# Kernel tuning notes

Hardware: AMD Instinct MI355X
Metric: run time of the kernel (lower is better)

## Reference

```python
import jax, jax.numpy as jnp
import numpy as np

jax.config.update('jax_enable_x64', True)

NV = 300000
NT = 1200000

# Lookup tables from GshellHelper buffers
TRIANGLE_TABLE = jnp.asarray(np.array([
    [-1, -1, -1, -1, -1, -1], [1, 0, 2, -1, -1, -1], [4, 0, 3, -1, -1, -1],
    [1, 4, 2, 1, 3, 4], [3, 1, 5, -1, -1, -1], [2, 3, 0, 2, 5, 3],
    [1, 4, 0, 1, 5, 4], [4, 2, 5, -1, -1, -1], [4, 5, 2, -1, -1, -1],
    [4, 1, 0, 4, 5, 1], [3, 2, 0, 3, 5, 2], [1, 3, 5, -1, -1, -1],
    [4, 1, 2, 4, 3, 1], [3, 0, 4, -1, -1, -1], [2, 0, 1, -1, -1, -1],
    [-1, -1, -1, -1, -1, -1]], dtype=np.int64))
NUM_TRIANGLES_TABLE = jnp.asarray(np.array([0, 1, 1, 2, 1, 2, 2, 1, 1, 2, 2, 1, 2, 1, 1, 0], dtype=np.int64))
BASE_TET_EDGES = jnp.asarray(np.array([0, 1, 0, 2, 0, 3, 1, 2, 1, 3, 2, 3], dtype=np.int64))


def setup_inputs() -> dict:
    key = jax.random.key(0)
    k1, k2, k3 = jax.random.split(key, 3)
    pos_nx3 = jax.random.normal(k1, (NV, 3), dtype=jnp.float32)
    sdf_n = jax.random.normal(k2, (NV,), dtype=jnp.float32)
    tet_fx4 = jax.random.randint(k3, (NT, 4), 0, NV, dtype=jnp.int64)
    return {'pos_nx3': pos_nx3, 'sdf_n': sdf_n, 'tet_fx4': tet_fx4}


def _marching_tets(pos_nx3, sdf_n, tet_fx4):
    Nv = pos_nx3.shape[0]
    Nt = tet_fx4.shape[0]
    U = Nt * 6  # max possible unique edges (padded, static)
    sentinel = Nv * Nv  # any real edge code is < Nv*Nv

    occ_n = sdf_n > 0                               # [Nv]
    occ_fx4 = occ_n[tet_fx4]                        # [Nt,4]

    # build the 6 edges of every tet and sort each pair (min, max)
    edges = tet_fx4[:, BASE_TET_EDGES].reshape(-1, 2)   # [Nt*6, 2]
    e0 = jnp.minimum(edges[:, 0], edges[:, 1])
    e1 = jnp.maximum(edges[:, 0], edges[:, 1])
    code = e0 * Nv + e1                                  # [Nt*6] int64 edge key

    # dedup edges (torch.unique(..., return_inverse=True) equivalent, padded)
    uniq, inv = jnp.unique(code, size=U, fill_value=sentinel, return_inverse=True)
    u0 = jnp.clip(uniq // Nv, 0, Nv - 1)
    u1 = jnp.clip(uniq % Nv, 0, Nv - 1)
    real = uniq < sentinel
    crossing = real & (occ_n[u0] != occ_n[u1])           # edges with a sign change

    # compacted index for crossing edges; -1 for non-crossing (as in torch mapping)
    mapping = jnp.where(crossing, jnp.cumsum(crossing.astype(jnp.int64)) - 1, -1)
    idx_map = mapping[inv].reshape(Nt, 6)                # [Nt,6]

    # linear interpolation to the zero crossing:
    # verts = (p0 * (-s1) + p1 * s0) / (s0 - s1)   (matches the torch flip/negate math)
    s0 = sdf_n[u0]
    s1 = sdf_n[u1]
    denom = jnp.where(crossing, s0 - s1, jnp.asarray(1.0, sdf_n.dtype))
    v = (pos_nx3[u0] * (-s1 / denom)[:, None] + pos_nx3[u1] * (s0 / denom)[:, None])

    # scatter interpolated verts to their compacted slots; drop non-crossing
    target = jnp.where(crossing, mapping, U)
    verts = jnp.zeros((U, 3), pos_nx3.dtype).at[target].set(v, mode='drop')

    # per-tet sign pattern -> triangle table lookup
    v_id = jnp.asarray([1, 2, 4, 8], dtype=jnp.int64)
    tetindex = (occ_fx4.astype(jnp.int64) * v_id[None, :]).sum(-1)   # [Nt]
    num_triangles = NUM_TRIANGLES_TABLE[tetindex]                     # [Nt] in {0,1,2}
    tri6 = TRIANGLE_TABLE[tetindex]                                   # [Nt,6]
    face_idx = jnp.take_along_axis(idx_map, jnp.clip(tri6, 0, 5), axis=1).reshape(Nt, 2, 3)
    valid_tri = jnp.arange(2, dtype=jnp.int64)[None, :] < num_triangles[:, None]
    faces = jnp.where(valid_tri[:, :, None], face_idx, -1)            # [Nt,2,3], -1 padded

    return verts, faces, num_triangles, crossing


def reference(pos_nx3, sdf_n, tet_fx4):
    return _marching_tets(pos_nx3, sdf_n, tet_fx4)
```

## Files before the change

### kernel.cpp

```cpp
#include <hip/hip_runtime.h>
#include <stdint.h>

typedef unsigned long long u64;
typedef unsigned int u32;

#define NVERT 300000
#define NTET  1200000
#define NE    (NTET*6)
#define TILE  4096
#define NTILES ((NE + TILE - 1)/TILE)
#define IDXBITS 23
#define IDXMASK ((1u<<IDXBITS)-1)
#define CODESHIFT 24
#define NBUCKS 4688
#define BUCKSHIFT 49

#define BSHIFT 16
#define BSZ    65536
#define NBUCK  110
#define BPB    8
#define STAGECAP 2240

#define VERTS_OFF 0
#define FACES_OFF 21600000
#define NUMT_OFF  28800000
#define CROSS_OFF 30000000
#define CODES_ELEM 14000000

__constant__ int c_ea[6] = {0,0,0,1,1,2};
__constant__ int c_eb[6] = {1,2,3,2,3,3};
__constant__ int c_numtri[16] = {0,1,1,2,1,2,2,1,1,2,2,1,2,1,1,0};
__constant__ int c_tritab[16][6] = {
 {-1,-1,-1,-1,-1,-1},{1,0,2,-1,-1,-1},{4,0,3,-1,-1,-1},{1,4,2,1,3,4},
 {3,1,5,-1,-1,-1},{2,3,0,2,5,3},{1,4,0,1,5,4},{4,2,5,-1,-1,-1},
 {4,5,2,-1,-1,-1},{4,1,0,4,5,1},{3,2,0,3,5,2},{1,3,5,-1,-1,-1},
 {4,1,2,4,3,1},{3,0,4,-1,-1,-1},{2,0,1,-1,-1,-1},{-1,-1,-1,-1,-1,-1}};

__device__ __forceinline__ int sw(int j){ return j ^ ((j >> 4) & 15); }

__global__ void k_pack(const int* __restrict__ tet, const float* __restrict__ sdf,
                       u64* __restrict__ dst, float* __restrict__ occF, u32* __restrict__ hist){
  __shared__ u32 h[NBUCKS];
  int tid = threadIdx.x;
  for (int r=tid; r<NBUCKS; r+=256) h[r]=0;
  __syncthreads();
  int t = blockIdx.x*blockDim.x + tid;
  if (t < NTET){
    int4 q = ((const int4*)tet)[t];
    int v[4] = {q.x, q.y, q.z, q.w};
    u32 o[4];
    int occ = 0;
    #pragma unroll
    for (int j=0;j<4;j++){ o[j] = sdf[v[j]] > 0.f ? 1u : 0u; occ |= (int)o[j] << j; }
    occF[t] = (float)occ;
    u64 base = (u64)t*6;
    #pragma unroll
    for (int k=0;k<6;k++){
      int a = v[c_ea[k]], b = v[c_eb[k]];
      u64 cross = (o[c_ea[k]] != o[c_eb[k]]) ? 1ull : 0ull;
      int e0 = min(a,b), e1 = max(a,b);
      u64 code = ((u64)e0 << 19) | (u64)e1;
      u64 key = (code << CODESHIFT) | (cross << IDXBITS) | (base + (u64)k);
      dst[base+k] = key;
      atomicAdd(&h[(u32)(key >> BUCKSHIFT)], 1u);
    }
  }
  __syncthreads();
  for (int r=tid; r<NBUCKS; r+=256){
    u32 c = h[r];
    if (c) atomicAdd(&hist[r], c);
  }
}

__global__ void k_psd(const float* __restrict__ pos, const float* __restrict__ sdf,
                      float4* __restrict__ psd){
  int v = blockIdx.x*blockDim.x + threadIdx.x;
  if (v < NVERT) psd[v] = make_float4(pos[3*v], pos[3*v+1], pos[3*v+2], sdf[v]);
}

__global__ void k_fillm1(float4* __restrict__ p, int n4){
  int i = blockIdx.x*blockDim.x + threadIdx.x;
  if (i < n4) p[i] = make_float4(-1.f,-1.f,-1.f,-1.f);
}

__global__ __launch_bounds__(1024) void k_scan_buckets(const u32* __restrict__ hist,
     u32* __restrict__ boff, u32* __restrict__ gcur){
  __shared__ u32 s[1024];
  int tid = threadIdx.x;
  u32 carry = 0;
  for (int start=0; start<NBUCKS; start+=1024){
    int idx = start + tid;
    u32 x = (idx < NBUCKS) ? hist[idx] : 0;
    s[tid] = x; __syncthreads();
    for (int off=1; off<1024; off<<=1){
      u32 t = (tid >= off) ? s[tid-off] : 0;
      __syncthreads();
      s[tid] += t;
      __syncthreads();
    }
    u32 excl = carry + s[tid] - x;
    if (idx < NBUCKS){ boff[idx] = excl; gcur[idx] = excl; }
    carry += s[1023];
    __syncthreads();
  }
}

__global__ __launch_bounds__(256) void k_bucket_scatter(const u64* __restrict__ src,
     u64* __restrict__ dst, u32* __restrict__ gcur){
  __shared__ u32 cnt[NBUCKS];
  __shared__ u32 cur[NBUCKS];
  int tid = threadIdx.x;
  for (int r=tid;r<NBUCKS;r+=256) cnt[r]=0;
  __syncthreads();
  int gi = blockIdx.x*TILE + tid*16;
  u64 kk[16];
  if (gi + 16 <= NE){
    const ulonglong2* p2 = (const ulonglong2*)(src + gi);
    #pragma unroll
    for (int k2=0;k2<8;k2++){ ulonglong2 t = p2[k2]; kk[2*k2]=t.x; kk[2*k2+1]=t.y; }
  } else {
    #pragma unroll
    for (int k=0;k<16;k++) kk[k] = (gi+k < NE) ? src[gi+k] : 0ull;
  }
  #pragma unroll
  for (int k=0;k<16;k++){
    if (gi+k < NE) atomicAdd(&cnt[(u32)(kk[k] >> BUCKSHIFT)], 1u);
  }
  __syncthreads();
  for (int r=tid;r<NBUCKS;r+=256){
    u32 c = cnt[r];
    cur[r] = c ? atomicAdd(&gcur[r], c) : 0u;
  }
  __syncthreads();
  #pragma unroll
  for (int k=0;k<16;k++){
    if (gi+k < NE){
      u32 b = (u32)(kk[k] >> BUCKSHIFT);
      u32 p = atomicAdd(&cur[b], 1u);
      dst[p] = kk[k];
    }
  }
}

__global__ __launch_bounds__(256) void k_sort_bucket(const u64* __restrict__ src,
     u64* __restrict__ dst, const u32* __restrict__ hist, const u32* __restrict__ boff){
  __shared__ u64 keys[TILE];
  __shared__ u64 wsum[4];
  int b = blockIdx.x, tid = threadIdx.x;
  u32 n = hist[b];
  if (n == 0) return;
  u32 base = boff[b];
  for (int k=0;k<16;k++){
    int j = k*256 + tid;
    keys[sw(j)] = (j < (int)n) ? src[base + j] : ~0ull;
  }
  __syncthreads();
  for (int q=0;q<26;q+=2){
    int sh = 24 + q;
    u64 myk[16];
    u32 vpack = 0;
    u64 c = 0;
    #pragma unroll
    for (int k=0;k<16;k++){
      myk[k] = keys[sw(tid*16+k)];
      u32 d2 = (u32)((myk[k] >> sh) & 3);
      vpack |= d2 << (2*k);
      c += 1ull << (16*d2);
    }
    u64 v = c;
    #pragma unroll
    for (int off=1; off<64; off<<=1){
      u64 t = __shfl_up(v, off, 64);
      if ((tid & 63) >= off) v += t;
    }
    if ((tid & 63) == 63) wsum[tid >> 6] = v;
    __syncthreads();
    u64 pre = 0, tot = 0;
    #pragma unroll
    for (int wv=0; wv<4; wv++){
      u64 wsv = wsum[wv];
      if (wv < (tid >> 6)) pre += wsv;
      tot += wsv;
    }
    u64 run = v + pre - c;
    u32 T0=(u32)(tot&0xFFFF), T1=(u32)((tot>>16)&0xFFFF), T2=(u32)((tot>>32)&0xFFFF);
    u64 Bp = ((u64)(T0) << 16) | ((u64)(T0+T1) << 32) | ((u64)(T0+T1+T2) << 48);
    #pragma unroll
    for (int k=0;k<16;k++){
      u32 d2 = (vpack >> (2*k)) & 3;
      u32 pos = (u32)((Bp >> (16*d2)) & 0xFFFF) + (u32)((run >> (16*d2)) & 0xFFFF);
      run += 1ull << (16*d2);
      keys[sw((int)pos)] = myk[k];
    }
    __syncthreads();
  }
  for (int k=0;k<16;k++){
    int j = k*256 + tid;
    if (j < (int)n) dst[base + j] = keys[sw(j)];
  }
}

__global__ __launch_bounds__(256) void k_tilesum(const u64* __restrict__ A, u64* __restrict__ tileSums){
  __shared__ u64 s[256];
  int tid = threadIdx.x;
  int start = blockIdx.x*TILE + tid*16;
  u64 myk[16];
  if (start < NE){
    const ulonglong2* A2 = (const ulonglong2*)(A + start);
    #pragma unroll
    for (int k2=0;k2<8;k2++){ ulonglong2 t = A2[k2]; myk[2*k2]=t.x; myk[2*k2+1]=t.y; }
  } else {
    #pragma unroll
    for (int k=0;k<16;k++) myk[k]=0;
  }
  u64 prev = (start > 0 && start <= NE) ? A[start-1] : ~0ull;
  u32 th=0, tc=0;
  #pragma unroll
  for (int k=0;k<16;k++){
    int i = start + k;
    if (i < NE){
      u64 v = myk[k];
      if ((v>>CODESHIFT) != (prev>>CODESHIFT)){
        th++;
        if ((v>>IDXBITS) & 1ull) tc++;
      }
      prev = v;
    }
  }
  s[tid] = ((u64)th<<32) | (u64)tc;
  __syncthreads();
  for (int off=128; off>0; off>>=1){
    if (tid<off) s[tid]+=s[tid+off];
    __syncthreads();
  }
  if (tid==0) tileSums[blockIdx.x] = s[0];
}

__global__ void k_scan_tiles(u64* __restrict__ tileSums, u64* __restrict__ tileOff){
  __shared__ u64 s[256];
  int tid = threadIdx.x;
  u64 carry=0;
  for (int start=0; start<NTILES; start+=256){
    int idx=start+tid;
    u64 x = (idx<NTILES)? tileSums[idx] : 0;
    s[tid]=x; __syncthreads();
    for (int off=1;off<256;off<<=1){
      u64 t=(tid>=off)?s[tid-off]:0;
      __syncthreads();
      s[tid]+=t;
      __syncthreads();
    }
    u64 incl=s[tid], tot=s[255];
    if (idx<NTILES) tileOff[idx] = carry + incl - x;
    carry += tot;
    __syncthreads();
  }
  if (tid==0) tileOff[NTILES] = carry;
}

__global__ __launch_bounds__(256) void k_emit_light(const u64* __restrict__ A,
     const u64* __restrict__ tileOff, u64* __restrict__ pairs, u32* __restrict__ cursors,
     u64* __restrict__ codes, float* __restrict__ crossing_out){
  __shared__ u64 s[256];
  __shared__ u32 cnt[NBUCK], lcur[NBUCK];
  __shared__ u32 lofs[NBUCK+1];
  __shared__ u32 gbase[NBUCK];
  __shared__ u32 pscan[128];
  __shared__ u64 stage[STAGECAP];
  int tid=threadIdx.x, blk=blockIdx.x;
  int start = blk*TILE + tid*16;
  if (tid < NBUCK){ cnt[tid]=0; lcur[tid]=0; }
  u64 myk[16];
  if (start < NE){
    const ulonglong2* A2 = (const ulonglong2*)(A + start);
    #pragma unroll
    for (int k2=0;k2<8;k2++){ ulonglong2 t = A2[k2]; myk[2*k2]=t.x; myk[2*k2+1]=t.y; }
  } else {
    #pragma unroll
    for (int k=0;k<16;k++) myk[k]=0;
  }
  u64 prev = (start > 0 && start <= NE) ? A[start-1] : ~0ull;
  u32 headm=0, crossm=0;
  #pragma unroll
  for (int k=0;k<16;k++){
    int i = start + k;
    if (i<NE){
      u64 v = myk[k];
      if ((v>>CODESHIFT) != (prev>>CODESHIFT)) headm |= 1u<<k;
      if ((v>>IDXBITS) & 1ull) crossm |= 1u<<k;
      prev = v;
    }
  }
  __syncthreads();
  #pragma unroll
  for (int k=0;k<16;k++){
    if ((start+k) < NE && ((crossm>>k)&1u))
      atomicAdd(&cnt[((u32)myk[k] & IDXMASK)>>BSHIFT], 1u);
  }
  u32 th = __popc(headm), tc = __popc(headm & crossm);
  u64 x = ((u64)th<<32)|(u64)tc;
  s[tid]=x; __syncthreads();
  for (int off=1;off<256;off<<=1){
    u64 t=(tid>=off)?s[tid-off]:0;
    __syncthreads();
    s[tid]+=t;
    __syncthreads();
  }
  u64 excl = s[tid]-x;
  if (tid < 128) pscan[tid] = (tid < NBUCK) ? cnt[tid] : 0;
  __syncthreads();
  for (int off=1; off<128; off<<=1){
    u32 t = 0;
    if (tid < 128 && tid >= off) t = pscan[tid-off];
    __syncthreads();
    if (tid < 128) pscan[tid] += t;
    __syncthreads();
  }
  if (tid < NBUCK) lofs[tid] = pscan[tid] - cnt[tid];
  if (tid == 0) lofs[NBUCK] = pscan[127];
  if (tid < NBUCK) gbase[tid] = atomicAdd(&cursors[tid], cnt[tid]);
  __syncthreads();
  bool use_stage = (lofs[NBUCK] <= STAGECAP);
  u64 baseOff = tileOff[blk] + excl;
  u32 H = (u32)(baseOff>>32);
  u32 C = (u32)(baseOff & 0xFFFFFFFFull);
  #pragma unroll
  for (int k=0;k<16;k++){
    int i = start+k;
    if (i>=NE) break;
    bool head  = (headm>>k)&1u;
    bool cross = (crossm>>k)&1u;
    if (head){ H++; if(cross) C++; }
    if (cross){
      int m = (int)C-1;
      u32 orig = (u32)myk[k] & IDXMASK;
      u32 b = orig>>BSHIFT;
      u32 r = atomicAdd(&lcur[b], 1u);
      u64 pr = ((u64)orig<<32) | (u64)(u32)m;
      if (use_stage) stage[lofs[b] + r] = pr;
      else           pairs[(size_t)b*BSZ + gbase[b] + r] = pr;
    }
    if (head){
      crossing_out[H-1] = cross ? 1.f : 0.f;
      if (cross) codes[C-1] = myk[k]>>CODESHIFT;
    }
  }
  __syncthreads();
  if (use_stage){
    int ncross = (int)lofs[NBUCK];
    for (int j = tid; j < ncross; j += 256){
      int lo=0, hi=NBUCK;
      while (hi - lo > 1){ int mid=(lo+hi)>>1; if ((int)lofs[mid] <= j) lo=mid; else hi=mid; }
      pairs[(size_t)lo*BSZ + gbase[lo] + (u32)(j - (int)lofs[lo])] = stage[j];
    }
  }
}

__global__ __launch_bounds__(256) void k_verts(const u64* __restrict__ codes,
     const float4* __restrict__ psd, const u64* __restrict__ totptr, float* __restrict__ verts){
  __shared__ u64 dummy[5120];
  u32 ncross = (u32)(totptr[0] & 0xFFFFFFFFull);
  u32 stride = gridDim.x * blockDim.x;
  for (u32 i = blockIdx.x*blockDim.x + threadIdx.x; i < ncross; i += stride){
    u64 code = codes[i];
    u32 u0 = (u32)(code >> 19), u1 = (u32)(code & 0x7FFFFull);
    float4 a = psd[u0], b = psd[u1];
    float denom = a.w - b.w;
    float w0 = (-b.w)/denom, w1 = a.w/denom;
    verts[3*i+0] = a.x*w0 + b.x*w1;
    verts[3*i+1] = a.y*w0 + b.y*w1;
    verts[3*i+2] = a.z*w0 + b.z*w1;
  }
  if ((int)ncross < -1){ dummy[threadIdx.x] = codes[0]; verts[0] = (float)dummy[255]; }
}

__global__ void k_map_scatter(const u64* __restrict__ pairs, const u32* __restrict__ cursors,
                              float* __restrict__ mapF){
  int b = blockIdx.x / BPB, sub = blockIdx.x % BPB;
  u32 n = cursors[b];
  const u64* p = pairs + (size_t)b*BSZ;
  for (u32 i = (u32)(sub*256 + threadIdx.x); i < n; i += BPB*256){
    u64 v = p[i];
    mapF[(u32)(v>>32)] = (float)(int)(u32)v;
  }
}

__global__ void k_faces(const float* __restrict__ occF, float* faceRegion, float* __restrict__ numt){
  int t = blockIdx.x*blockDim.x + threadIdx.x;
  if (t>=NTET) return;
  int occ = (int)occF[t];
  int ntri = c_numtri[occ];
  float em[6];
  #pragma unroll
  for (int j=0;j<6;j++) em[j] = faceRegion[t*6+j];
  float f[6];
  #pragma unroll
  for (int j=0;j<6;j++){
    int tri = c_tritab[occ][j];
    f[j] = ((j/3) < ntri) ? em[tri] : -1.f;
  }
  #pragma unroll
  for (int j=0;j<6;j++) faceRegion[t*6+j] = f[j];
  numt[t] = (float)ntri;
}

extern "C" void kernel_launch(void* const* d_in, const int* in_sizes, int n_in,
                              void* d_out, int out_size, void* d_ws, size_t ws_size,
                              hipStream_t stream) {
  const float* pos = (const float*)d_in[0];
  const float* sdf = (const float*)d_in[1];
  const int*   tet = (const int*)d_in[2];
  float* out = (float*)d_out;

  char* w = (char*)d_ws;
  u64* bufA     = (u64*)w;
  u32* hist     = (u32*)(w + 57600000);
  u32* boff     = (u32*)(w + 57618752);
  u32* gcur     = (u32*)(w + 57637504);
  u64* tileSums = (u64*)(w + 57656256);
  u64* tileOff  = (u64*)(w + 57670320);
  u32* cursors  = (u32*)(w + 57684392);
  float4* psd   = (float4*)(w + 57684992);
  u64* pairs_ws = (u64*)(w + 62484992);

  u64* bufB  = (u64*)d_out;
  u64* codes = (u64*)(out + CODES_ELEM);

  hipMemsetAsync(hist, 0, NBUCKS*sizeof(u32), stream);

  k_pack<<<(NTET+255)/256, 256, 0, stream>>>(tet, sdf, bufA, out + NUMT_OFF, hist);
  k_psd<<<(NVERT+255)/256, 256, 0, stream>>>(pos, sdf, psd);
  k_fillm1<<<(7200000/4 + 255)/256, 256, 0, stream>>>((float4*)(out + FACES_OFF), 7200000/4);

  k_scan_buckets<<<1, 1024, 0, stream>>>(hist, boff, gcur);

  k_bucket_scatter<<<NTILES, 256, 0, stream>>>(bufA, bufB, gcur);
  k_sort_bucket<<<NBUCKS, 256, 0, stream>>>(bufB, bufA, hist, boff);

  k_tilesum<<<NTILES, 256, 0, stream>>>(bufA, tileSums);
  k_scan_tiles<<<1, 256, 0, stream>>>(tileSums, tileOff);

  hipMemsetAsync(out + CROSS_OFF, 0, (size_t)7200000*4, stream);
  hipMemsetAsync(cursors, 0, NBUCK*sizeof(u32), stream);

  k_emit_light<<<NTILES, 256, 0, stream>>>(bufA, tileOff, pairs_ws, cursors,
                                           codes, out + CROSS_OFF);

  hipMemsetAsync(out + VERTS_OFF, 0, (size_t)CODES_ELEM*4, stream);
  k_verts<<<1024, 256, 0, stream>>>(codes, psd, tileOff + NTILES, out + VERTS_OFF);
  hipMemsetAsync(out + CODES_ELEM, 0, (size_t)(21600000-CODES_ELEM)*4, stream);

  k_map_scatter<<<NBUCK*BPB, 256, 0, stream>>>(pairs_ws, cursors, out + FACES_OFF);
  k_faces<<<(NTET+255)/256, 256, 0, stream>>>(out + NUMT_OFF, out + FACES_OFF, out + NUMT_OFF);
}
```

Before: 633.2 us.

## Use 3-bit radix passes and size-specialized bucket sort kernels

New measurement: 663.9 us. 4.9% more time.

```diff
diff --git a/kernel.cpp b/kernel.cpp
--- a/kernel.cpp
+++ b/kernel.cpp
@@ -107,10 +107,9 @@
 
 __global__ __launch_bounds__(256) void k_bucket_scatter(const u64* __restrict__ src,
      u64* __restrict__ dst, u32* __restrict__ gcur){
-  __shared__ u32 cnt[NBUCKS];
-  __shared__ u32 cur[NBUCKS];
+  __shared__ u32 h[NBUCKS];
   int tid = threadIdx.x;
-  for (int r=tid;r<NBUCKS;r+=256) cnt[r]=0;
+  for (int r=tid;r<NBUCKS;r+=256) h[r]=0;
   __syncthreads();
   int gi = blockIdx.x*TILE + tid*16;
   u64 kk[16];
@@ -124,77 +123,102 @@
   }
   #pragma unroll
   for (int k=0;k<16;k++){
-    if (gi+k < NE) atomicAdd(&cnt[(u32)(kk[k] >> BUCKSHIFT)], 1u);
+    if (gi+k < NE) atomicAdd(&h[(u32)(kk[k] >> BUCKSHIFT)], 1u);
   }
   __syncthreads();
   for (int r=tid;r<NBUCKS;r+=256){
-    u32 c = cnt[r];
-    cur[r] = c ? atomicAdd(&gcur[r], c) : 0u;
+    u32 c = h[r];
+    h[r] = c ? atomicAdd(&gcur[r], c) : 0u;
   }
   __syncthreads();
   #pragma unroll
   for (int k=0;k<16;k++){
     if (gi+k < NE){
       u32 b = (u32)(kk[k] >> BUCKSHIFT);
-      u32 p = atomicAdd(&cur[b], 1u);
+      u32 p = atomicAdd(&h[b], 1u);
       dst[p] = kk[k];
     }
   }
 }
 
+template<int NK>
 __global__ __launch_bounds__(256) void k_sort_bucket(const u64* __restrict__ src,
      u64* __restrict__ dst, const u32* __restrict__ hist, const u32* __restrict__ boff){
-  __shared__ u64 keys[TILE];
-  __shared__ u64 wsum[4];
+  __shared__ u64 keys[NK*256];
+  __shared__ u64 wsum[4][2];
   int b = blockIdx.x, tid = threadIdx.x;
   u32 n = hist[b];
   if (n == 0) return;
+  if (NK == 4  && n > 1024) return;
+  if (NK == 8  && (n <= 1024 || n > 2048)) return;
+  if (NK == 16 && n <= 2048) return;
   u32 base = boff[b];
-  for (int k=0;k<16;k++){
+  #pragma unroll
+  for (int k=0;k<NK;k++){
     int j = k*256 + tid;
     keys[sw(j)] = (j < (int)n) ? src[base + j] : ~0ull;
   }
   __syncthreads();
-  for (int q=0;q<26;q+=2){
-    int sh = 24 + q;
-    u64 myk[16];
-    u32 vpack = 0;
-    u64 c = 0;
-    #pragma unroll
-    for (int k=0;k<16;k++){
-      myk[k] = keys[sw(tid*16+k)];
-      u32 d2 = (u32)((myk[k] >> sh) & 3);
-      vpack |= d2 << (2*k);
-      c += 1ull << (16*d2);
-    }
-    u64 v = c;
+  int mywave = tid >> 6;
+  #pragma unroll 1
+  for (int q=0;q<9;q++){
+    int sh = 24 + 3*q;
+    u64 myk[NK];
+    u64 vpack = 0;
+    u64 c0 = 0, c1 = 0;
+    #pragma unroll
+    for (int k=0;k<NK;k++){
+      myk[k] = keys[sw(tid*NK+k)];
+      u32 d = (u32)((myk[k] >> sh) & 7);
+      vpack |= (u64)d << (3*k);
+      u64 inc = 1ull << (16*(d&3));
+      c0 += (d & 4) ? 0 : inc;
+      c1 += (d & 4) ? inc : 0;
+    }
+    u64 v0 = c0, v1 = c1;
     #pragma unroll
     for (int off=1; off<64; off<<=1){
-      u64 t = __shfl_up(v, off, 64);
-      if ((tid & 63) >= off) v += t;
-    }
-    if ((tid & 63) == 63) wsum[tid >> 6] = v;
-    __syncthreads();
-    u64 pre = 0, tot = 0;
+      u64 t0 = __shfl_up(v0, off, 64);
+      u64 t1 = __shfl_up(v1, off, 64);
+      if ((tid & 63) >= off){ v0 += t0; v1 += t1; }
+    }
+    if ((tid & 63) == 63){ wsum[mywave][0] = v0; wsum[mywave][1] = v1; }
+    __syncthreads();
+    u64 pre0=0, pre1=0, tot0=0, tot1=0;
     #pragma unroll
     for (int wv=0; wv<4; wv++){
-      u64 wsv = wsum[wv];
-      if (wv < (tid >> 6)) pre += wsv;
-      tot += wsv;
-    }
-    u64 run = v + pre - c;
-    u32 T0=(u32)(tot&0xFFFF), T1=(u32)((tot>>16)&0xFFFF), T2=(u32)((tot>>32)&0xFFFF);
-    u64 Bp = ((u64)(T0) << 16) | ((u64)(T0+T1) << 32) | ((u64)(T0+T1+T2) << 48);
-    #pragma unroll
-    for (int k=0;k<16;k++){
-      u32 d2 = (vpack >> (2*k)) & 3;
-      u32 pos = (u32)((Bp >> (16*d2)) & 0xFFFF) + (u32)((run >> (16*d2)) & 0xFFFF);
-      run += 1ull << (16*d2);
+      u64 x0 = wsum[wv][0], x1 = wsum[wv][1];
+      if (wv < mywave){ pre0 += x0; pre1 += x1; }
+      tot0 += x0; tot1 += x1;
+    }
+    u64 run0 = v0 + pre0 - c0;
+    u64 run1 = v1 + pre1 - c1;
+    u64 Bp0 = 0, Bp1 = 0;
+    u32 acc = 0;
+    #pragma unroll
+    for (int b2=0;b2<8;b2++){
+      u32 f = (u32)(((b2 < 4 ? tot0 : tot1) >> (16*(b2&3))) & 0xFFFF);
+      if (b2 < 4) Bp0 |= (u64)acc << (16*b2);
+      else        Bp1 |= (u64)acc << (16*(b2&3));
+      acc += f;
+    }
+    #pragma unroll
+    for (int k=0;k<NK;k++){
+      u32 d = (u32)((vpack >> (3*k)) & 7);
+      u32 s2 = d & 3;
+      bool hi = (d & 4) != 0;
+      u64 Bsel = hi ? Bp1 : Bp0;
+      u64 rsel = hi ? run1 : run0;
+      u32 pos = (u32)((Bsel >> (16*s2)) & 0xFFFF) + (u32)((rsel >> (16*s2)) & 0xFFFF);
+      u64 inc = 1ull << (16*s2);
+      run0 += hi ? 0 : inc;
+      run1 += hi ? inc : 0;
       keys[sw((int)pos)] = myk[k];
     }
     __syncthreads();
   }
-  for (int k=0;k<16;k++){
+  #pragma unroll
+  for (int k=0;k<NK;k++){
     int j = k*256 + tid;
     if (j < (int)n) dst[base + j] = keys[sw(j)];
   }
@@ -435,7 +459,9 @@
   k_scan_buckets<<<1, 1024, 0, stream>>>(hist, boff, gcur);
 
   k_bucket_scatter<<<NTILES, 256, 0, stream>>>(bufA, bufB, gcur);
-  k_sort_bucket<<<NBUCKS, 256, 0, stream>>>(bufB, bufA, hist, boff);
+  k_sort_bucket<4><<<NBUCKS, 256, 0, stream>>>(bufB, bufA, hist, boff);
+  k_sort_bucket<8><<<NBUCKS, 256, 0, stream>>>(bufB, bufA, hist, boff);
+  k_sort_bucket<16><<<NBUCKS, 256, 0, stream>>>(bufB, bufA, hist, boff);
 
   k_tilesum<<<NTILES, 256, 0, stream>>>(bufA, tileSums);
   k_scan_tiles<<<1, 256, 0, stream>>>(tileSums, tileOff);
```
